# Kernel tuning notes

Hardware: AMD Instinct MI355X
Metric: run time of the kernel (lower is better)

The kernel has to match this reference:

```python
import jax, jax.numpy as jnp
import numpy as np
from math import ceil

B, T, FQ, D = 2, 48, 100, 512
H, DFF, L, WSZ = 8, 2048, 6, 8


def setup_inputs() -> dict:
    key = jax.random.key(0)
    ks = jax.random.split(key, 8)
    g = lambda k, shape: jax.random.normal(k, shape, jnp.float32) * 0.02
    return {
        "frame_queries": jax.random.normal(ks[0], (B, T, FQ, D), jnp.float32),
        "Wp": g(ks[1], (D, D)), "bp": jnp.zeros((D,), jnp.float32),
        "Wqkv": g(ks[2], (L, 3 * D, D)), "bqkv": jnp.zeros((L, 3 * D), jnp.float32),
        "Wo": g(ks[3], (L, D, D)), "bo": jnp.zeros((L, D), jnp.float32),
        "ln1_s": jnp.ones((L, D), jnp.float32), "ln1_b": jnp.zeros((L, D), jnp.float32),
        "W1": g(ks[4], (L, DFF, D)), "b1": jnp.zeros((L, DFF), jnp.float32),
        "W2": g(ks[5], (L, D, DFF)), "b2": jnp.zeros((L, D), jnp.float32),
        "ln2_s": jnp.ones((L, D), jnp.float32), "ln2_b": jnp.zeros((L, D), jnp.float32),
    }


def _ln(x, s, b, eps=1e-5):
    mu = x.mean(-1, keepdims=True)
    var = ((x - mu) ** 2).mean(-1, keepdims=True)
    return (x - mu) * jax.lax.rsqrt(var + eps) * s + b


def _mha(x, Wqkv_i, bqkv_i, Wo_i, bo_i, add_mask):
    # x: [Bw, S, C]; add_mask: None or [Bw, 1, S, S] additive float
    Bw, S, C = x.shape
    hd = C // H
    qkv = x @ Wqkv_i.T + bqkv_i
    q, k, v = jnp.split(qkv, 3, axis=-1)
    q = q.reshape(Bw, S, H, hd).transpose(0, 2, 1, 3)
    k = k.reshape(Bw, S, H, hd).transpose(0, 2, 1, 3)
    v = v.reshape(Bw, S, H, hd).transpose(0, 2, 1, 3)
    scores = jnp.einsum('bhqd,bhkd->bhqk', q, k) * jnp.float32(1.0 / np.sqrt(hd))
    if add_mask is not None:
        scores = scores + add_mask
    a = jax.nn.softmax(scores, axis=-1)
    o = jnp.einsum('bhqk,bhkd->bhqd', a, v).transpose(0, 2, 1, 3).reshape(Bw, S, C)
    return o @ Wo_i.T + bo_i


def _shift_mask():
    # padding mask is all-False (T % WSZ == 0), faithful construction of the
    # shifted-window additive mask as in the torch code.
    Nw = T // WSZ
    half = int(ceil(WSZ / 2))
    S = WSZ * FQ
    am = jnp.zeros((B, T), dtype=bool)
    r = jnp.roll(am, half, axis=1).reshape(B, Nw, WSZ)
    m = jnp.broadcast_to(r[..., None], (B, Nw, WSZ, WSZ))
    m = m.at[:, 0].set(m[:, 0] | m[:, 0].swapaxes(-1, -2))
    m = m.at[:, -1].set(m[:, -1] | m[:, -1].swapaxes(-1, -2))
    m = m.at[:, 0, :half, half:].set(True)
    m = m.at[:, 0, half:, :half].set(True)
    mfull = jnp.broadcast_to(m.reshape(B * Nw, WSZ, 1, WSZ, 1),
                             (B * Nw, WSZ, FQ, WSZ, FQ)).reshape(B * Nw, S, S)
    return (mfull.astype(jnp.float32) * -1000.0)[:, None]  # [B*Nw,1,S,S]


def reference(frame_queries, Wp, bp, Wqkv, bqkv, Wo, bo, ln1_s, ln1_b,
              W1, b1, W2, b2, ln2_s, ln2_b):
    Nw = T // WSZ
    half = int(ceil(WSZ / 2))
    S = WSZ * FQ
    x = frame_queries @ Wp.T + bp  # [B, T, FQ, D]
    shift_add = _shift_mask()
    for i in range(L):
        if i % 2 == 0:
            # plain window attention
            xw = x.reshape(B * Nw, S, D)
            xw = _ln(xw + _mha(xw, Wqkv[i], bqkv[i], Wo[i], bo[i], None),
                     ln1_s[i], ln1_b[i])
            x = xw.reshape(B, T, FQ, D)
        else:
            # shifted window attention
            xs = jnp.roll(x, half, axis=1)
            xw = xs.reshape(B * Nw, S, D)
            xw = _ln(xw + _mha(xw, Wqkv[i], bqkv[i], Wo[i], bo[i], shift_add),
                     ln1_s[i], ln1_b[i])
            x = jnp.roll(xw.reshape(B, T, FQ, D), -half, axis=1)
        # FFN (pointwise over channel dim)
        h = jax.nn.relu(x @ W1[i].T + b1[i]) @ W2[i].T + b2[i]
        x = _ln(x + h, ln2_s[i], ln2_b[i])
    return x  # [B, T, FQ, D] == 'lb t nq c'
```

## Files before the change

### kernel.cpp

```cpp
#include <hip/hip_runtime.h>


typedef float  f4    __attribute__((ext_vector_type(4)));
typedef __bf16 bf8   __attribute__((ext_vector_type(8)));
typedef unsigned short u16x8 __attribute__((ext_vector_type(8)));
typedef unsigned short u16x4 __attribute__((ext_vector_type(4)));
typedef unsigned int   u32x2 __attribute__((ext_vector_type(2)));
typedef unsigned int   u32x4 __attribute__((ext_vector_type(4)));

__device__ __forceinline__ unsigned short f2bf(float f) {
    unsigned int u = __builtin_bit_cast(unsigned int, f);
    u += 0x7fffu + ((u >> 16) & 1u);
    return (unsigned short)(u >> 16);
}
__device__ __forceinline__ float bf2f(unsigned short s) {
    return __builtin_bit_cast(float, ((unsigned int)s) << 16);
}

#define GLD16(gp, lp) __builtin_amdgcn_global_load_lds( \
    (const __attribute__((address_space(1))) void*)(gp), \
    (__attribute__((address_space(3))) void*)(lp), 16, 0, 0)

__device__ __forceinline__ int map_row(int r, int rshift) {
    if (!rshift) return r;
    int bb = r / 4800, rem = r % 4800;
    int tt = rem / 100, f = rem - tt * 100;
    return bb * 4800 + ((tt + rshift) % 48) * 100 + f;
}

template<int BM>
__global__ __launch_bounds__(256) void mfma_gemm(
    const unsigned short* __restrict__ A, const unsigned short* __restrict__ W,
    const float* __restrict__ bias, float* Cf, unsigned short* Cb,
    int M, int N, int K, int relu, int rshift, int qscale, int NB)
{
    constexpr int MI      = BM / 32;
    constexpr int ABUF    = BM * 32;
    constexpr int SB      = ABUF + 4096;
    constexpr int AROUNDS = BM / 64;
    __shared__ unsigned short Ls[3 * SB];
    const int tid = threadIdx.x, lane = tid & 63, wave = tid >> 6;

    const int per = gridDim.x >> 3;
    const int l = (blockIdx.x & 7) * per + (blockIdx.x >> 3);
    const int MB = M / BM;
    if (l >= NB * MB) return;
    const int n0 = (l % NB) * 128, m0 = (l / NB) * BM;

    const unsigned short* ga[AROUNDS];
    #pragma unroll
    for (int it = 0; it < AROUNDS; ++it) {
        int s = it * 256 + tid, row = s >> 2, cg = (s & 3) ^ ((row >> 1) & 3);
        ga[it] = A + (size_t)map_row(m0 + row, rshift) * K + cg * 8;
    }
    const unsigned short* gb[2];
    #pragma unroll
    for (int it = 0; it < 2; ++it) {
        int s = it * 256 + tid, row = s >> 2, cg = (s & 3) ^ ((row >> 1) & 3);
        gb[it] = W + (size_t)(n0 + row) * K + cg * 8;
    }

    const int wm = (wave >> 1) * (BM / 2), wn = (wave & 1) * 64;
    const int lr = lane & 15, quad = lane >> 4;

    auto STAGE = [&](int kt2, int buf) {
        const int k1 = kt2 << 5;
        unsigned short* Lb = &Ls[buf * SB];
        #pragma unroll
        for (int it = 0; it < AROUNDS; ++it)
            GLD16(ga[it] + k1, &Lb[(it * 256 + wave * 64) * 8]);
        #pragma unroll
        for (int it = 0; it < 2; ++it)
            GLD16(gb[it] + k1, &Lb[ABUF + (it * 256 + wave * 64) * 8]);
    };

    f4 acc[MI][4];
    #pragma unroll
    for (int i = 0; i < MI; ++i)
        #pragma unroll
        for (int j = 0; j < 4; ++j) acc[i][j] = 0.f;

    const int NK = K >> 5;
    STAGE(0, 0);
    STAGE(1, 1);

    int cb = 0;
    for (int kt = 0; kt < NK; ++kt) {
        if (kt + 1 < NK) {
            if constexpr (BM == 128) asm volatile("s_waitcnt vmcnt(4)" ::: "memory");
            else                     asm volatile("s_waitcnt vmcnt(3)" ::: "memory");
        } else {
            asm volatile("s_waitcnt vmcnt(0)" ::: "memory");
        }
        __builtin_amdgcn_s_barrier();
        __builtin_amdgcn_sched_barrier(0);
        const int ib = (cb == 0) ? 2 : cb - 1;
        if (kt + 2 < NK) STAGE(kt + 2, ib);

        const unsigned short* Ab = &Ls[cb * SB];
        const unsigned short* Bb = &Ls[cb * SB + ABUF];
        bf8 af[MI], bfr[4];
        #pragma unroll
        for (int mi = 0; mi < MI; ++mi) {
            int m = wm + mi * 16 + lr;
            int c = quad ^ ((m >> 1) & 3);
            af[mi] = __builtin_bit_cast(bf8, *(const u16x8*)&Ab[(m * 4 + c) * 8]);
        }
        #pragma unroll
        for (int ni = 0; ni < 4; ++ni) {
            int n = wn + ni * 16 + lr;
            int c = quad ^ ((n >> 1) & 3);
            bfr[ni] = __builtin_bit_cast(bf8, *(const u16x8*)&Bb[(n * 4 + c) * 8]);
        }
        #pragma unroll
        for (int mi = 0; mi < MI; ++mi)
            #pragma unroll
            for (int ni = 0; ni < 4; ++ni)
                acc[mi][ni] = __builtin_amdgcn_mfma_f32_16x16x32_bf16(
                    af[mi], bfr[ni], acc[mi][ni], 0, 0, 0);
        __builtin_amdgcn_sched_barrier(0);
        cb = (cb + 1 == 3) ? 0 : cb + 1;
    }

    #pragma unroll
    for (int mi = 0; mi < MI; ++mi) {
        #pragma unroll
        for (int ni = 0; ni < 4; ++ni) {
            const int rowg = m0 + wm + mi * 16 + quad * 4;
            const int colg = n0 + wn + ni * 16 + lr;
            const float bv = bias[colg];
            const float sc = (qscale && colg < 512) ? 0.125f : 1.0f;
            #pragma unroll
            for (int r = 0; r < 4; ++r) {
                float v = (acc[mi][ni][r] + bv) * sc;
                if (relu) v = fmaxf(v, 0.f);
                const size_t off = (size_t)(rowg + r) * N + colg;
                if (Cf) Cf[off] = v;
                if (Cb) Cb[off] = f2bf(v);
            }
        }
    }
}

template<int BM>
__global__ __launch_bounds__(256) void gemm_bk64(
    const unsigned short* __restrict__ A, const unsigned short* __restrict__ W,
    const float* __restrict__ bias, float* Cf, unsigned short* Cb,
    int M, int N, int K, int relu, int rshift, int qscale)
{
    constexpr int MI      = BM / 32;
    constexpr int ABUF    = BM * 64;
    constexpr int AROUNDS = BM / 32;
    __shared__ unsigned short As[2 * ABUF];
    __shared__ unsigned short Bs[2 * 8192];
    const int tid = threadIdx.x, lane = tid & 63, wave = tid >> 6;
    const int n0 = blockIdx.x * 128, m0 = blockIdx.y * BM;

    const unsigned short* ga[AROUNDS];
    unsigned short* la[AROUNDS];
    #pragma unroll
    for (int it = 0; it < AROUNDS; ++it) {
        int s = it * 256 + tid, row = s >> 3, cg = (s & 7) ^ (row & 7);
        ga[it] = A + (size_t)map_row(m0 + row, rshift) * K + cg * 8;
        la[it] = &As[(it * 256 + wave * 64) * 8];
    }
    const unsigned short* gb[4];
    unsigned short* lb[4];
    #pragma unroll
    for (int it = 0; it < 4; ++it) {
        int s = it * 256 + tid, row = s >> 3, cg = (s & 7) ^ (row & 7);
        gb[it] = W + (size_t)(n0 + row) * K + cg * 8;
        lb[it] = &Bs[(it * 256 + wave * 64) * 8];
    }

    const int wm = (wave >> 1) * (BM / 2), wn = (wave & 1) * 64;
    const int lr = lane & 15, quad = lane >> 4;

    f4 acc[MI][4];
    #pragma unroll
    for (int i = 0; i < MI; ++i)
        #pragma unroll
        for (int j = 0; j < 4; ++j) acc[i][j] = 0.f;

    #pragma unroll
    for (int it = 0; it < AROUNDS; ++it) GLD16(ga[it], la[it]);
    #pragma unroll
    for (int it = 0; it < 4; ++it) GLD16(gb[it], lb[it]);

    const int NK = K >> 6;
    for (int kt = 0; kt < NK; ++kt) {
        const int cb = kt & 1, nb = cb ^ 1;
        __syncthreads();
        if (kt + 1 < NK) {
            const int k1 = (kt + 1) << 6;
            #pragma unroll
            for (int it = 0; it < AROUNDS; ++it) GLD16(ga[it] + k1, la[it] + nb * ABUF);
            #pragma unroll
            for (int it = 0; it < 4; ++it)       GLD16(gb[it] + k1, lb[it] + nb * 8192);
        }
        const unsigned short* Ab = &As[cb * ABUF];
        const unsigned short* Bb = &Bs[cb * 8192];
        #pragma unroll
        for (int kh = 0; kh < 2; ++kh) {
            bf8 af[MI], bfr[4];
            #pragma unroll
            for (int mi = 0; mi < MI; ++mi) {
                int m = wm + mi * 16 + lr;
                int c = (kh * 4 + quad) ^ (m & 7);
                af[mi] = __builtin_bit_cast(bf8, *(const u16x8*)&Ab[(m * 8 + c) * 8]);
            }
            #pragma unroll
            for (int ni = 0; ni < 4; ++ni) {
                int n = wn + ni * 16 + lr;
                int c = (kh * 4 + quad) ^ (n & 7);
                bfr[ni] = __builtin_bit_cast(bf8, *(const u16x8*)&Bb[(n * 8 + c) * 8]);
            }
            #pragma unroll
            for (int mi = 0; mi < MI; ++mi)
                #pragma unroll
                for (int ni = 0; ni < 4; ++ni)
                    acc[mi][ni] = __builtin_amdgcn_mfma_f32_16x16x32_bf16(
                        af[mi], bfr[ni], acc[mi][ni], 0, 0, 0);
        }
    }

    #pragma unroll
    for (int mi = 0; mi < MI; ++mi) {
        #pragma unroll
        for (int ni = 0; ni < 4; ++ni) {
            const int rowg = m0 + wm + mi * 16 + quad * 4;
            const int colg = n0 + wn + ni * 16 + lr;
            const float bv = bias[colg];
            const float sc = (qscale && colg < 512) ? 0.125f : 1.0f;
            #pragma unroll
            for (int r = 0; r < 4; ++r) {
                float v = (acc[mi][ni][r] + bv) * sc;
                if (relu) v = fmaxf(v, 0.f);
                const size_t off = (size_t)(rowg + r) * N + colg;
                if (Cf) Cf[off] = v;
                if (Cb) Cb[off] = f2bf(v);
            }
        }
    }
}

__global__ __launch_bounds__(320) void flash_attn_mfma(
    const unsigned short* __restrict__ qkv, unsigned short* __restrict__ o,
    int masked)
{
    __shared__ unsigned short Ks[2][2048];
    __shared__ __align__(16) unsigned short VTs[2][2048];
    __shared__ unsigned short Ps[5][576];

    const int bid = blockIdx.x;
    const int h = bid & 7, kk2 = bid >> 3;
    const int qt = kk2 % 10, w = kk2 / 10;
    const int tid = threadIdx.x, lane = tid & 63, wave = tid >> 6;
    const int lr = lane & 15, quad = lane >> 4;
    const int qb = qt * 80 + wave * 16;
    const size_t wbase = (size_t)w * 800 * 1536;
    const bool do_mask = masked && ((w % 6) == 0);

    bf8 aQ[2];
    {
        const unsigned short* qp =
            qkv + wbase + (size_t)(qb + lr) * 1536 + h * 64 + quad * 8;
        aQ[0] = __builtin_bit_cast(bf8, *(const u16x8*)qp);
        aQ[1] = __builtin_bit_cast(bf8, *(const u16x8*)(qp + 32));
    }

    const unsigned short* gk = qkv;
    int kw = 0;
    if (wave < 4) {
        int s = wave * 64 + lane, row = s >> 3, clog = (s & 7) ^ (row & 7);
        gk = qkv + wbase + (size_t)row * 1536 + 512 + h * 64 + clog * 8;
        kw = wave * 512;
    }
    const unsigned short* gvp = qkv;
    if (wave < 4) {
        int c = wave * 64 + lane, S = c >> 3, wc = c & 7;
        int vkey = 8 * (S & 3) + 4 * ((S >> 2) & 1) + (wc >> 1);
        int vdim = 16 * (S >> 3) + 8 * (wc & 1);
        gvp = qkv + wbase + (size_t)vkey * 1536 + 1024 + h * 64 + vdim;
    }

    unsigned vtb;
    {
        auto p3 = (__attribute__((address_space(3))) unsigned short*)&VTs[0][0];
        vtb = (unsigned)(unsigned long long)p3 + (unsigned)(lane << 3);
    }

    float lsum = 0.f;
    f4 oacc[4];
    #pragma unroll
    for (int dt = 0; dt < 4; ++dt) oacc[dt] = 0.f;

    const bool qhl = (qb + lr) >= 400;

    if (wave < 4) {
        GLD16(gk, &Ks[0][kw]);
        GLD16(gvp, &VTs[0][wave * 512]);
    }

    for (int kt = 0; kt < 25; ++kt) {
        const int cb = kt & 1, nb = cb ^ 1;
        const int k0 = kt * 32;
        __syncthreads();

        const bool pf = (kt < 24);
        if (pf && wave < 4) {
            GLD16(gk  + (size_t)(k0 + 32) * 1536, &Ks[nb][kw]);
            GLD16(gvp + (size_t)(k0 + 32) * 1536, &VTs[nb][wave * 512]);
        }

        f4 st[2];
        st[0] = 0.f; st[1] = 0.f;
        __builtin_amdgcn_s_setprio(1);
        #pragma unroll
        for (int kh = 0; kh < 2; ++kh) {
            const int cx = (kh * 4 + quad) ^ (lane & 7);
            bf8 kf0 = __builtin_bit_cast(bf8, *(const u16x8*)&Ks[cb][(lr * 8 + cx) * 8]);
            bf8 kf1 = __builtin_bit_cast(bf8, *(const u16x8*)&Ks[cb][((16 + lr) * 8 + cx) * 8]);
            st[0] = __builtin_amdgcn_mfma_f32_16x16x32_bf16(kf0, aQ[kh], st[0], 0, 0, 0);
            st[1] = __builtin_amdgcn_mfma_f32_16x16x32_bf16(kf1, aQ[kh], st[1], 0, 0, 0);
        }
        __builtin_amdgcn_s_setprio(0);

        {
            u16x4 pk0, pk1;
            float ls = 0.f;
            #pragma unroll
            for (int r = 0; r < 4; ++r) {
                float a = st[0][r], b = st[1][r];
                if (do_mask) {
                    if (((k0 + quad * 4 + r) >= 400) != qhl)      a -= 1000.f;
                    if (((k0 + 16 + quad * 4 + r) >= 400) != qhl) b -= 1000.f;
                }
                float p0 = __expf(fminf(a, 80.f));
                float p1 = __expf(fminf(b, 80.f));
                ls += p0 + p1;
                pk0[r] = (unsigned short)(__builtin_bit_cast(unsigned int, p0) >> 16);
                pk1[r] = (unsigned short)(__builtin_bit_cast(unsigned int, p1) >> 16);
            }
            lsum += ls;
            *(u16x4*)&Ps[wave][lr * 36 + quad * 4]      = pk0;
            *(u16x4*)&Ps[wave][lr * 36 + 16 + quad * 4] = pk1;
        }

        bf8 aP = __builtin_bit_cast(bf8, *(const u16x8*)&Ps[wave][lr * 36 + quad * 8]);
        const unsigned va = vtb + ((unsigned)cb << 12);
        u32x2 t0, t1, t2, t3, t4, t5, t6, t7;
        asm volatile("ds_read_b64_tr_b16 %0, %1"             : "=v"(t0) : "v"(va));
        asm volatile("ds_read_b64_tr_b16 %0, %1 offset:512"  : "=v"(t1) : "v"(va));
        asm volatile("ds_read_b64_tr_b16 %0, %1 offset:1024" : "=v"(t2) : "v"(va));
        asm volatile("ds_read_b64_tr_b16 %0, %1 offset:1536" : "=v"(t3) : "v"(va));
        asm volatile("ds_read_b64_tr_b16 %0, %1 offset:2048" : "=v"(t4) : "v"(va));
        asm volatile("ds_read_b64_tr_b16 %0, %1 offset:2560" : "=v"(t5) : "v"(va));
        asm volatile("ds_read_b64_tr_b16 %0, %1 offset:3072" : "=v"(t6) : "v"(va));
        asm volatile("ds_read_b64_tr_b16 %0, %1 offset:3584" : "=v"(t7) : "v"(va));
        asm volatile("s_waitcnt lgkmcnt(0)" ::: "memory");
        __builtin_amdgcn_sched_barrier(0);
        __builtin_amdgcn_s_setprio(1);
        {
            u32x4 b0 = {t0[0], t0[1], t1[0], t1[1]};
            u32x4 b1 = {t2[0], t2[1], t3[0], t3[1]};
            u32x4 b2 = {t4[0], t4[1], t5[0], t5[1]};
            u32x4 b3 = {t6[0], t6[1], t7[0], t7[1]};
            oacc[0] = __builtin_amdgcn_mfma_f32_16x16x32_bf16(aP, __builtin_bit_cast(bf8, b0), oacc[0], 0, 0, 0);
            oacc[1] = __builtin_amdgcn_mfma_f32_16x16x32_bf16(aP, __builtin_bit_cast(bf8, b1), oacc[1], 0, 0, 0);
            oacc[2] = __builtin_amdgcn_mfma_f32_16x16x32_bf16(aP, __builtin_bit_cast(bf8, b2), oacc[2], 0, 0, 0);
            oacc[3] = __builtin_amdgcn_mfma_f32_16x16x32_bf16(aP, __builtin_bit_cast(bf8, b3), oacc[3], 0, 0, 0);
        }
        __builtin_amdgcn_s_setprio(0);
    }

    {
        float l = lsum;
        l += __shfl_xor(l, 16);
        l += __shfl_xor(l, 32);
        float inv[4];
        #pragma unroll
        for (int r = 0; r < 4; ++r)
            inv[r] = 1.0f / __shfl(l, quad * 4 + r);
        #pragma unroll
        for (int dt = 0; dt < 4; ++dt)
            #pragma unroll
            for (int r = 0; r < 4; ++r)
                o[((size_t)w * 800 + qb + quad * 4 + r) * 512 + h * 64 + dt * 16 + lr] =
                    f2bf(oacc[dt][r] * inv[r]);
    }
}

__global__ __launch_bounds__(256) void add_ln_kernel(
    const unsigned short* xb, const unsigned short* dlt,
    const float* __restrict__ s, const float* __restrict__ b,
    float* outf, unsigned short* outb, int rshift)
{
    const int wave = threadIdx.x >> 6, lane = threadIdx.x & 63;
    const int row = blockIdx.x * 4 + wave;
    const int xrow = map_row(row, rshift);
    const int c = lane * 8;
    u16x8 xv = *(const u16x8*)(xb  + (size_t)xrow * 512 + c);
    u16x8 dv = *(const u16x8*)(dlt + (size_t)row  * 512 + c);
    f4 u0, u1;
    #pragma unroll
    for (int j = 0; j < 4; ++j) {
        u0[j] = bf2f(xv[j])     + bf2f(dv[j]);
        u1[j] = bf2f(xv[4 + j]) + bf2f(dv[4 + j]);
    }
    float sum = u0[0]+u0[1]+u0[2]+u0[3] + u1[0]+u1[1]+u1[2]+u1[3];
    #pragma unroll
    for (int o2 = 1; o2 < 64; o2 <<= 1) sum += __shfl_xor(sum, o2);
    const float mu = sum * (1.0f / 512.0f);
    f4 d0 = u0 - mu, d1 = u1 - mu;
    float sq = d0[0]*d0[0]+d0[1]*d0[1]+d0[2]*d0[2]+d0[3]*d0[3]
             + d1[0]*d1[0]+d1[1]*d1[1]+d1[2]*d1[2]+d1[3]*d1[3];
    #pragma unroll
    for (int o2 = 1; o2 < 64; o2 <<= 1) sq += __shfl_xor(sq, o2);
    const float rs = rsqrtf(sq * (1.0f / 512.0f) + 1e-5f);
    f4 s0 = *(const f4*)(s + c), s1 = *(const f4*)(s + c + 4);
    f4 b0 = *(const f4*)(b + c), b1 = *(const f4*)(b + c + 4);
    f4 y0, y1;
    #pragma unroll
    for (int j = 0; j < 4; ++j) { y0[j] = d0[j]*rs*s0[j]+b0[j]; y1[j] = d1[j]*rs*s1[j]+b1[j]; }
    u16x8 ob;
    #pragma unroll
    for (int j = 0; j < 4; ++j) { ob[j] = f2bf(y0[j]); ob[4+j] = f2bf(y1[j]); }
    *(u16x8*)(outb + (size_t)xrow * 512 + c) = ob;
    if (outf) {
        float* of = outf + (size_t)xrow * 512 + c;
        *(f4*)of = y0; *(f4*)(of + 4) = y1;
    }
}

__global__ __launch_bounds__(256) void cast_f2b_kernel(
    const float* __restrict__ in, unsigned short* __restrict__ out, int n4)
{
    const int i = blockIdx.x * 256 + threadIdx.x;
    if (i >= n4) return;
    f4 v = ((const f4*)in)[i];
    u16x4 o4 = {f2bf(v[0]), f2bf(v[1]), f2bf(v[2]), f2bf(v[3])};
    ((u16x4*)out)[i] = o4;
}

extern "C" void kernel_launch(void* const* d_in, const int* in_sizes, int n_in,
                              void* d_out, int out_size, void* d_ws, size_t ws_size,
                              hipStream_t stream)
{
    const float* fq   = (const float*)d_in[0];
    const float* Wp   = (const float*)d_in[1];
    const float* bp   = (const float*)d_in[2];
    const float* Wqkv = (const float*)d_in[3];
    const float* bqkv = (const float*)d_in[4];
    const float* Wo   = (const float*)d_in[5];
    const float* bo   = (const float*)d_in[6];
    const float* l1s  = (const float*)d_in[7];
    const float* l1b  = (const float*)d_in[8];
    const float* W1   = (const float*)d_in[9];
    const float* b1   = (const float*)d_in[10];
    const float* W2   = (const float*)d_in[11];
    const float* b2   = (const float*)d_in[12];
    const float* l2s  = (const float*)d_in[13];
    const float* l2b  = (const float*)d_in[14];
    float* out = (float*)d_out;

    unsigned short* xb   = (unsigned short*)d_ws;
    unsigned short* qkvb = xb + 4915200;
    unsigned short* hbuf = qkvb + 14745600;
    unsigned short* wbuf = hbuf + 19660800;
    unsigned short* obuf = hbuf;
    unsigned short* t1b  = qkvb;
    unsigned short* fqb  = hbuf;
    unsigned short* wqA = wbuf;
    unsigned short* woA = wqA + 4718592;
    unsigned short* w1A = woA + 1572864;
    unsigned short* w2A = w1A + 6291456;
    unsigned short* wpA = w2A + 6291456;

    const dim3 blk(256);
    #define G8(n) dim3((((n) + 7) & ~7))
    cast_f2b_kernel<<<dim3(4800), blk, 0, stream>>>(fq,   fqb, 1228800);
    cast_f2b_kernel<<<dim3(4608), blk, 0, stream>>>(Wqkv, wqA, 1179648);
    cast_f2b_kernel<<<dim3(1536), blk, 0, stream>>>(Wo,   woA, 393216);
    cast_f2b_kernel<<<dim3(6144), blk, 0, stream>>>(W1,   w1A, 1572864);
    cast_f2b_kernel<<<dim3(6144), blk, 0, stream>>>(W2,   w2A, 1572864);
    cast_f2b_kernel<<<dim3(256),  blk, 0, stream>>>(Wp,   wpA, 65536);
    mfma_gemm<64><<<G8(600), blk, 0, stream>>>(fqb, wpA, bp, nullptr, xb,
                                               9600, 512, 512, 0, 0, 0, 4);

    for (int i = 0; i < 6; ++i) {
        const int rsh = (i & 1) ? 44 : 0;
        const unsigned short* wq = wqA + (size_t)i * 786432;
        const unsigned short* wo = woA + (size_t)i * 262144;
        const unsigned short* w1 = w1A + (size_t)i * 1048576;
        const unsigned short* w2 = w2A + (size_t)i * 1048576;
        mfma_gemm<128><<<G8(900), blk, 0, stream>>>(xb, wq, bqkv + i * 1536,
                                                    nullptr, qkvb, 9600, 1536, 512, 0, rsh, 1, 12);
        flash_attn_mfma<<<dim3(960), dim3(320), 0, stream>>>(qkvb, obuf, i & 1);
        mfma_gemm<64><<<G8(600), blk, 0, stream>>>(obuf, wo, bo + i * 512,
                                                   nullptr, t1b, 9600, 512, 512, 0, 0, 0, 4);
        add_ln_kernel<<<dim3(2400), blk, 0, stream>>>(xb, t1b, l1s + i * 512, l1b + i * 512,
                                                      nullptr, xb, rsh);
        gemm_bk64<128><<<dim3(16, 75), blk, 0, stream>>>(xb, w1, b1 + i * 2048,
                                                         nullptr, hbuf, 9600, 2048, 512, 1, 0, 0);
        gemm_bk64<64><<<dim3(4, 150), blk, 0, stream>>>(hbuf, w2, b2 + i * 512,
                                                        nullptr, t1b, 9600, 512, 2048, 0, 0, 0);
        add_ln_kernel<<<dim3(2400), blk, 0, stream>>>(xb, t1b, l2s + i * 512, l2b + i * 512,
                                                      (i == 5) ? out : nullptr, xb, 0);
    }
    #undef G8
}
```

Before: 1.159 ms.

## Shrink attention blocks to two waves and merge weight casts into one kernel

The flash attention kernel now runs 2400 blocks of 128 threads, each covering 32 queries, instead of 960 blocks of 320 threads covering 80 queries. Every thread now issues two K and two V async loads per tile, where before only four of five waves did loads. The aim is more blocks and better occupancy and balance across CUs, at the cost of reloading K/V more often per query. The six separate fp32-to-bf16 cast launches are also merged into one launch, which saves launch overhead.

Result: slower. 1.237 ms (+6.8%).

```diff
diff --git a/kernel.cpp b/kernel.cpp
--- a/kernel.cpp
+++ b/kernel.cpp
@@ -244,20 +244,20 @@
     }
 }
 
-__global__ __launch_bounds__(320) void flash_attn_mfma(
+__global__ __launch_bounds__(128) void flash_attn_mfma(
     const unsigned short* __restrict__ qkv, unsigned short* __restrict__ o,
     int masked)
 {
     __shared__ unsigned short Ks[2][2048];
     __shared__ __align__(16) unsigned short VTs[2][2048];
-    __shared__ unsigned short Ps[5][576];
+    __shared__ unsigned short Ps[2][576];
 
     const int bid = blockIdx.x;
-    const int h = bid & 7, kk2 = bid >> 3;
-    const int qt = kk2 % 10, w = kk2 / 10;
+    const int h = bid & 7, r2 = bid >> 3;
+    const int qt = r2 % 25, w = r2 / 25;
     const int tid = threadIdx.x, lane = tid & 63, wave = tid >> 6;
     const int lr = lane & 15, quad = lane >> 4;
-    const int qb = qt * 80 + wave * 16;
+    const int qb = qt * 32 + wave * 16;
     const size_t wbase = (size_t)w * 800 * 1536;
     const bool do_mask = masked && ((w % 6) == 0);
 
@@ -269,20 +269,19 @@
         aQ[1] = __builtin_bit_cast(bf8, *(const u16x8*)(qp + 32));
     }
 
-    const unsigned short* gk = qkv;
-    int kw = 0;
-    if (wave < 4) {
-        int s = wave * 64 + lane, row = s >> 3, clog = (s & 7) ^ (row & 7);
-        gk = qkv + wbase + (size_t)row * 1536 + 512 + h * 64 + clog * 8;
-        kw = wave * 512;
-    }
-    const unsigned short* gvp = qkv;
-    if (wave < 4) {
-        int c = wave * 64 + lane, S = c >> 3, wc = c & 7;
+    const int c0 = tid, c1 = 128 + tid;
+    const unsigned short* gk0 = qkv + wbase + (size_t)(c0 >> 3) * 1536 + 512
+                              + h * 64 + ((c0 & 7) ^ ((c0 >> 3) & 7)) * 8;
+    const unsigned short* gk1 = qkv + wbase + (size_t)(c1 >> 3) * 1536 + 512
+                              + h * 64 + ((c1 & 7) ^ ((c1 >> 3) & 7)) * 8;
+    auto vsrc = [&](int c) {
+        int S = c >> 3, wc = c & 7;
         int vkey = 8 * (S & 3) + 4 * ((S >> 2) & 1) + (wc >> 1);
         int vdim = 16 * (S >> 3) + 8 * (wc & 1);
-        gvp = qkv + wbase + (size_t)vkey * 1536 + 1024 + h * 64 + vdim;
-    }
+        return qkv + wbase + (size_t)vkey * 1536 + 1024 + h * 64 + vdim;
+    };
+    const unsigned short* gv0 = vsrc(c0);
+    const unsigned short* gv1 = vsrc(c1);
 
     unsigned vtb;
     {
@@ -297,20 +296,22 @@
 
     const bool qhl = (qb + lr) >= 400;
 
-    if (wave < 4) {
-        GLD16(gk, &Ks[0][kw]);
-        GLD16(gvp, &VTs[0][wave * 512]);
-    }
+    GLD16(gk0, &Ks[0][(wave * 64) * 8]);
+    GLD16(gk1, &Ks[0][(128 + wave * 64) * 8]);
+    GLD16(gv0, &VTs[0][(wave * 64) * 8]);
+    GLD16(gv1, &VTs[0][(128 + wave * 64) * 8]);
 
     for (int kt = 0; kt < 25; ++kt) {
         const int cb = kt & 1, nb = cb ^ 1;
         const int k0 = kt * 32;
         __syncthreads();
 
-        const bool pf = (kt < 24);
-        if (pf && wave < 4) {
-            GLD16(gk  + (size_t)(k0 + 32) * 1536, &Ks[nb][kw]);
-            GLD16(gvp + (size_t)(k0 + 32) * 1536, &VTs[nb][wave * 512]);
+        if (kt < 24) {
+            const size_t adv = (size_t)(k0 + 32) * 1536;
+            GLD16(gk0 + adv, &Ks[nb][(wave * 64) * 8]);
+            GLD16(gk1 + adv, &Ks[nb][(128 + wave * 64) * 8]);
+            GLD16(gv0 + adv, &VTs[nb][(wave * 64) * 8]);
+            GLD16(gv1 + adv, &VTs[nb][(128 + wave * 64) * 8]);
         }
 
         f4 st[2];
@@ -433,14 +434,25 @@
     }
 }
 
-__global__ __launch_bounds__(256) void cast_f2b_kernel(
-    const float* __restrict__ in, unsigned short* __restrict__ out, int n4)
+__global__ __launch_bounds__(256) void cast_all_kernel(
+    const float* __restrict__ fq,  const float* __restrict__ Wqkv,
+    const float* __restrict__ Wo,  const float* __restrict__ W1,
+    const float* __restrict__ W2,  const float* __restrict__ Wp,
+    unsigned short* fqb, unsigned short* wqA, unsigned short* woA,
+    unsigned short* w1A, unsigned short* w2A, unsigned short* wpA)
 {
-    const int i = blockIdx.x * 256 + threadIdx.x;
-    if (i >= n4) return;
-    f4 v = ((const f4*)in)[i];
+    int i = blockIdx.x * 256 + threadIdx.x;
+    const float* src; unsigned short* dst;
+    if (i < 1228800)                       { src = fq;   dst = fqb; }
+    else if ((i -= 1228800) < 1179648)     { src = Wqkv; dst = wqA; }
+    else if ((i -= 1179648) < 393216)      { src = Wo;   dst = woA; }
+    else if ((i -= 393216) < 1572864)      { src = W1;   dst = w1A; }
+    else if ((i -= 1572864) < 1572864)     { src = W2;   dst = w2A; }
+    else if ((i -= 1572864) < 65536)       { src = Wp;   dst = wpA; }
+    else return;
+    f4 v = ((const f4*)src)[i];
     u16x4 o4 = {f2bf(v[0]), f2bf(v[1]), f2bf(v[2]), f2bf(v[3])};
-    ((u16x4*)out)[i] = o4;
+    ((u16x4*)dst)[i] = o4;
 }
 
 extern "C" void kernel_launch(void* const* d_in, const int* in_sizes, int n_in,
@@ -479,12 +491,8 @@
 
     const dim3 blk(256);
     #define G8(n) dim3((((n) + 7) & ~7))
-    cast_f2b_kernel<<<dim3(4800), blk, 0, stream>>>(fq,   fqb, 1228800);
-    cast_f2b_kernel<<<dim3(4608), blk, 0, stream>>>(Wqkv, wqA, 1179648);
-    cast_f2b_kernel<<<dim3(1536), blk, 0, stream>>>(Wo,   woA, 393216);
-    cast_f2b_kernel<<<dim3(6144), blk, 0, stream>>>(W1,   w1A, 1572864);
-    cast_f2b_kernel<<<dim3(6144), blk, 0, stream>>>(W2,   w2A, 1572864);
-    cast_f2b_kernel<<<dim3(256),  blk, 0, stream>>>(Wp,   wpA, 65536);
+    cast_all_kernel<<<dim3(23488), blk, 0, stream>>>(fq, Wqkv, Wo, W1, W2, Wp,
+                                                     fqb, wqA, woA, w1A, w2A, wpA);
     mfma_gemm<64><<<G8(600), blk, 0, stream>>>(fqb, wpA, bp, nullptr, xb,
                                                9600, 512, 512, 0, 0, 0, 4);
 
@@ -496,7 +504,7 @@
         const unsigned short* w2 = w2A + (size_t)i * 1048576;
         mfma_gemm<128><<<G8(900), blk, 0, stream>>>(xb, wq, bqkv + i * 1536,
                                                     nullptr, qkvb, 9600, 1536, 512, 0, rsh, 1, 12);
-        flash_attn_mfma<<<dim3(960), dim3(320), 0, stream>>>(qkvb, obuf, i & 1);
+        flash_attn_mfma<<<dim3(2400), dim3(128), 0, stream>>>(qkvb, obuf, i & 1);
         mfma_gemm<64><<<G8(600), blk, 0, stream>>>(obuf, wo, bo + i * 512,
                                                    nullptr, t1b, 9600, 512, 512, 0, 0, 0, 4);
         add_ln_kernel<<<dim3(2400), blk, 0, stream>>>(xb, t1b, l1s + i * 512, l1b + i * 512,
```
